# Performance work log

Hardware: AMD Instinct MI355X
Metric: run time of the kernel (lower is better)

The kernel has to match this reference:

```python
import jax, jax.numpy as jnp
import numpy as np

N_NODES = 100000
N_EDGES = 1600000
N_GRAPHS = 2048
F_IN = 33
D = 256


def _graph_conv(x, edge_index, w_rel, b_rel, w_root):
    # PyG GraphConv (aggr='add'): out = lin_rel(sum_j x_j) + lin_root(x)
    src, dst = edge_index[0], edge_index[1]
    agg = jax.ops.segment_sum(x[src], dst, num_segments=x.shape[0])  # [N, F]
    return agg @ w_rel + b_rel + x @ w_root


def setup_inputs() -> dict:
    key = jax.random.key(0)
    ks = jax.random.split(key, 16)
    scale_in = 1.0 / np.sqrt(F_IN)
    scale_d = 1.0 / np.sqrt(D)
    inp = {
        "x": jax.random.normal(ks[0], (N_NODES, F_IN), dtype=jnp.float32),
        "edge_index": jax.random.randint(ks[1], (2, N_EDGES), 0, N_NODES),
        "batch_index": jnp.sort(jax.random.randint(ks[2], (N_NODES,), 0, N_GRAPHS)),
        # initial_conv: GraphConv(F_IN -> D)
        "w_rel0": jax.random.normal(ks[3], (F_IN, D), dtype=jnp.float32) * scale_in,
        "b_rel0": jnp.zeros((D,), dtype=jnp.float32),
        "w_root0": jax.random.normal(ks[4], (F_IN, D), dtype=jnp.float32) * scale_in,
        # conv1..conv3: GraphConv(D -> D)
        "w_rel1": jax.random.normal(ks[5], (D, D), dtype=jnp.float32) * scale_d,
        "b_rel1": jnp.zeros((D,), dtype=jnp.float32),
        "w_root1": jax.random.normal(ks[6], (D, D), dtype=jnp.float32) * scale_d,
        "w_rel2": jax.random.normal(ks[7], (D, D), dtype=jnp.float32) * scale_d,
        "b_rel2": jnp.zeros((D,), dtype=jnp.float32),
        "w_root2": jax.random.normal(ks[8], (D, D), dtype=jnp.float32) * scale_d,
        "w_rel3": jax.random.normal(ks[9], (D, D), dtype=jnp.float32) * scale_d,
        "b_rel3": jnp.zeros((D,), dtype=jnp.float32),
        "w_root3": jax.random.normal(ks[10], (D, D), dtype=jnp.float32) * scale_d,
        # output head Linear(D -> 1)
        "w_out": jax.random.normal(ks[11], (D, 1), dtype=jnp.float32) * scale_d,
        "b_out": jnp.zeros((1,), dtype=jnp.float32),
    }
    return inp


def reference(x, edge_index, batch_index,
              w_rel0, b_rel0, w_root0,
              w_rel1, b_rel1, w_root1,
              w_rel2, b_rel2, w_root2,
              w_rel3, b_rel3, w_root3,
              w_out, b_out):
    # dropout omitted (eval mode)
    h = jax.nn.gelu(_graph_conv(x, edge_index, w_rel0, b_rel0, w_root0))
    h = jax.nn.gelu(_graph_conv(h, edge_index, w_rel1, b_rel1, w_root1))
    h = jax.nn.gelu(_graph_conv(h, edge_index, w_rel2, b_rel2, w_root2))
    h = jax.nn.gelu(_graph_conv(h, edge_index, w_rel3, b_rel3, w_root3))
    # global mean pool over graphs
    sums = jax.ops.segment_sum(h, batch_index, num_segments=N_GRAPHS)          # [G, D]
    counts = jax.ops.segment_sum(jnp.ones((h.shape[0],), h.dtype), batch_index,
                                 num_segments=N_GRAPHS)                         # [G]
    pooled = sums / jnp.maximum(counts, 1.0)[:, None]
    return pooled @ w_out + b_out                                               # [G, 1]
```

## Files before the change

kernel.cpp:

```cpp
#include <hip/hip_runtime.h>
#include <math.h>

#define NN 100000
#define NE 1600000
#define NG 2048
#define FIN 33
#define DD 256

#define SH 8
#define NB ((NN + 255) >> 8)
#define CH 4096
#define PCAP 4608
#define ESCAP 6144

typedef __attribute__((ext_vector_type(8))) short bf16x8;
typedef __attribute__((ext_vector_type(4))) float f32x4;

__device__ __forceinline__ float b2f(unsigned short u){
    union { unsigned int i; float f; } c; c.i = ((unsigned int)u) << 16; return c.f;
}
__device__ __forceinline__ unsigned short f2b(float f){
    union { float f; unsigned int u; } c; c.f = f;
    unsigned int r = c.u + 0x7fffu + ((c.u >> 16) & 1u);
    return (unsigned short)(r >> 16);
}

__device__ __forceinline__ float gelu_tanh(float x){
    float x3 = x * x * x;
    float t = tanhf(0.7978845608028654f * (x + 0.044715f * x3));
    return 0.5f * x * (1.0f + t);
}

__global__ __launch_bounds__(256) void k_bin(const int* __restrict__ src,
                                             const int* __restrict__ dst,
                                             int* __restrict__ gcur,
                                             int2* __restrict__ pairs){
    __shared__ int cnt[NB];
    __shared__ int lb[NB];
    __shared__ int gbase[NB];
    __shared__ int sc[512];
    __shared__ int2 stage[CH];

    int t = threadIdx.x;
    for(int i = t; i < NB; i += 256) cnt[i] = 0;
    __syncthreads();

    int e0 = blockIdx.x * CH;
    int n = NE - e0; if(n > CH) n = CH;

    int  myb[16];
    int  myr[16];
    int2 myp[16];
    #pragma unroll
    for(int k = 0; k < 16; k++){
        int e = e0 + t + k * 256;
        if(e < NE){
            int s = src[e], d = dst[e];
            int b = d >> SH;
            myr[k] = atomicAdd(&cnt[b], 1);
            myb[k] = b;
            myp[k] = make_int2(s, d);
        } else myb[k] = -1;
    }
    __syncthreads();

    sc[t]       = (t       < NB) ? cnt[t]       : 0;
    sc[t + 256] = (t + 256 < NB) ? cnt[t + 256] : 0;
    __syncthreads();
    for(int off = 1; off < 512; off <<= 1){
        int a  = (t >= off)       ? sc[t - off]       : 0;
        int b2 = (t + 256 >= off) ? sc[t + 256 - off] : 0;
        __syncthreads();
        sc[t] += a; sc[t + 256] += b2;
        __syncthreads();
    }
    for(int i = t; i < NB; i += 256){
        lb[i] = sc[i] - cnt[i];
        int c = cnt[i];
        gbase[i] = (c > 0) ? atomicAdd(&gcur[i], c) : 0;
    }
    __syncthreads();

    #pragma unroll
    for(int k = 0; k < 16; k++){
        if(myb[k] >= 0) stage[lb[myb[k]] + myr[k]] = myp[k];
    }
    __syncthreads();

    for(int i = t; i < n; i += 256){
        int2 p = stage[i];
        int b = p.y >> SH;
        int tgt = gbase[b] + (i - lb[b]);
        if(tgt < PCAP) pairs[(size_t)b * PCAP + tgt] = p;
    }
}

__global__ void k_sscan(const int* __restrict__ gcur, int* __restrict__ boff){
    __shared__ int s[512];
    int t = threadIdx.x;
    int v = 0;
    if(t < NB){ v = gcur[t]; if(v > PCAP) v = PCAP; }
    s[t] = v; __syncthreads();
    for(int off = 1; off < 512; off <<= 1){
        int u = (t >= off) ? s[t - off] : 0;
        __syncthreads();
        s[t] += u;
        __syncthreads();
    }
    if(t < NB) boff[t] = s[t] - v;
}

__global__ __launch_bounds__(256) void k_bcsr(const int2* __restrict__ pairs,
                                              const int* __restrict__ gcur,
                                              const int* __restrict__ boff,
                                              int* __restrict__ deg,
                                              int* __restrict__ rs,
                                              int* __restrict__ esrc){
    __shared__ int hist[256];
    __shared__ int sc[256];
    __shared__ int cur2[256];
    __shared__ int est[ESCAP];

    int b = blockIdx.x;
    int t = threadIdx.x;
    int m = gcur[b]; if(m > PCAP) m = PCAP;
    int pstart = boff[b];
    const int2* bp = pairs + (size_t)b * PCAP;

    hist[t] = 0;
    __syncthreads();
    for(int i = t; i < m; i += 256) atomicAdd(&hist[bp[i].y & 255], 1);
    __syncthreads();

    sc[t] = hist[t]; __syncthreads();
    for(int off = 1; off < 256; off <<= 1){
        int u = (t >= off) ? sc[t - off] : 0;
        __syncthreads();
        sc[t] += u;
        __syncthreads();
    }
    int excl = sc[t] - hist[t];
    cur2[t] = excl;
    int node = (b << 8) + t;
    if(node < NN){
        deg[node] = hist[t];
        rs[node]  = pstart + excl;
    }
    __syncthreads();

    for(int i = t; i < m; i += 256){
        int2 p = bp[i];
        int pos = atomicAdd(&cur2[p.y & 255], 1);
        if(pos < ESCAP) est[pos] = p.x;
        else esrc[pstart + pos] = p.x;
    }
    __syncthreads();
    int lim = (m < ESCAP) ? m : ESCAP;
    for(int i = t; i < lim; i += 256) esrc[pstart + i] = est[i];
}

__global__ void k_xpad(const float* __restrict__ x, unsigned short* __restrict__ xb){
    int idx = blockIdx.x * 256 + threadIdx.x;
    if(idx >= NN * 64) return;
    int n = idx >> 6, c = idx & 63;
    xb[idx] = (c < FIN) ? f2b(x[(size_t)n * FIN + c]) : 0;
}

__global__ void k_aggx(const unsigned short* __restrict__ xb, const int* __restrict__ rs,
                       const int* __restrict__ deg, const int* __restrict__ esrc,
                       unsigned short* __restrict__ axb){
    int wv = (blockIdx.x * blockDim.x + threadIdx.x) >> 6;
    int lane = threadIdx.x & 63;
    int node = wv * 4 + (lane >> 4);
    int l16 = lane & 15;
    if(node >= NN) return;
    int start = rs[node], cnt = deg[node];
    float a0 = 0.f, a1 = 0.f, a2 = 0.f, a3 = 0.f;
    const unsigned short* xp = xb + l16 * 4;
    int j = 0;
    for(; j + 4 <= cnt; j += 4){
        int e0 = esrc[start+j], e1 = esrc[start+j+1], e2 = esrc[start+j+2], e3 = esrc[start+j+3];
        ushort4 v0 = *(const ushort4*)(xp + (size_t)e0 * 64);
        ushort4 v1 = *(const ushort4*)(xp + (size_t)e1 * 64);
        ushort4 v2 = *(const ushort4*)(xp + (size_t)e2 * 64);
        ushort4 v3 = *(const ushort4*)(xp + (size_t)e3 * 64);
        a0 += (b2f(v0.x) + b2f(v1.x)) + (b2f(v2.x) + b2f(v3.x));
        a1 += (b2f(v0.y) + b2f(v1.y)) + (b2f(v2.y) + b2f(v3.y));
        a2 += (b2f(v0.z) + b2f(v1.z)) + (b2f(v2.z) + b2f(v3.z));
        a3 += (b2f(v0.w) + b2f(v1.w)) + (b2f(v2.w) + b2f(v3.w));
    }
    for(; j < cnt; j++){
        int e = esrc[start + j];
        ushort4 v = *(const ushort4*)(xp + (size_t)e * 64);
        a0 += b2f(v.x); a1 += b2f(v.y); a2 += b2f(v.z); a3 += b2f(v.w);
    }
    ushort4 o; o.x = f2b(a0); o.y = f2b(a1); o.z = f2b(a2); o.w = f2b(a3);
    *(ushort4*)(axb + (size_t)node * 64 + l16 * 4) = o;
}

__global__ void k_agg256(const unsigned short* __restrict__ h, const int* __restrict__ rs,
                         const int* __restrict__ deg, const int* __restrict__ esrc,
                         unsigned short* __restrict__ agg){
    int w = (blockIdx.x * blockDim.x + threadIdx.x) >> 6;
    int lane = threadIdx.x & 63;
    if(w >= NN) return;
    int start = rs[w], cnt = deg[w];
    float a0 = 0.f, a1 = 0.f, a2 = 0.f, a3 = 0.f;
    const unsigned short* hp = h + lane * 4;
    int j = 0;
    for(; j + 8 <= cnt; j += 8){
        int e0 = esrc[start+j+0], e1 = esrc[start+j+1], e2 = esrc[start+j+2], e3 = esrc[start+j+3];
        int e4 = esrc[start+j+4], e5 = esrc[start+j+5], e6 = esrc[start+j+6], e7 = esrc[start+j+7];
        ushort4 v0 = *(const ushort4*)(hp + (size_t)e0 * DD);
        ushort4 v1 = *(const ushort4*)(hp + (size_t)e1 * DD);
        ushort4 v2 = *(const ushort4*)(hp + (size_t)e2 * DD);
        ushort4 v3 = *(const ushort4*)(hp + (size_t)e3 * DD);
        ushort4 v4 = *(const ushort4*)(hp + (size_t)e4 * DD);
        ushort4 v5 = *(const ushort4*)(hp + (size_t)e5 * DD);
        ushort4 v6 = *(const ushort4*)(hp + (size_t)e6 * DD);
        ushort4 v7 = *(const ushort4*)(hp + (size_t)e7 * DD);
        a0 += ((b2f(v0.x)+b2f(v1.x)) + (b2f(v2.x)+b2f(v3.x))) + ((b2f(v4.x)+b2f(v5.x)) + (b2f(v6.x)+b2f(v7.x)));
        a1 += ((b2f(v0.y)+b2f(v1.y)) + (b2f(v2.y)+b2f(v3.y))) + ((b2f(v4.y)+b2f(v5.y)) + (b2f(v6.y)+b2f(v7.y)));
        a2 += ((b2f(v0.z)+b2f(v1.z)) + (b2f(v2.z)+b2f(v3.z))) + ((b2f(v4.z)+b2f(v5.z)) + (b2f(v6.z)+b2f(v7.z)));
        a3 += ((b2f(v0.w)+b2f(v1.w)) + (b2f(v2.w)+b2f(v3.w))) + ((b2f(v4.w)+b2f(v5.w)) + (b2f(v6.w)+b2f(v7.w)));
    }
    for(; j < cnt; j++){
        int s = esrc[start + j];
        ushort4 v = *(const ushort4*)(hp + (size_t)s * DD);
        a0 += b2f(v.x); a1 += b2f(v.y); a2 += b2f(v.z); a3 += b2f(v.w);
    }
    ushort4 o; o.x = f2b(a0); o.y = f2b(a1); o.z = f2b(a2); o.w = f2b(a3);
    *(ushort4*)(agg + (size_t)w * DD + lane * 4) = o;
}

__global__ void k_wt(const float* __restrict__ W, unsigned short* __restrict__ Bt){
    __shared__ float s[16][17];
    int tx = threadIdx.x, ty = threadIdx.y;
    int k = blockIdx.y * 16 + ty;
    int j = blockIdx.x * 16 + tx;
    s[ty][tx] = W[k * DD + j];
    __syncthreads();
    Bt[(size_t)(blockIdx.x * 16 + ty) * DD + blockIdx.y * 16 + tx] = f2b(s[tx][ty]);
}

__global__ void k_wt0(const float* __restrict__ W, unsigned short* __restrict__ Bt){
    int idx = blockIdx.x * 256 + threadIdx.x;
    if(idx >= DD * 64) return;
    int j = idx >> 6, k = idx & 63;
    Bt[idx] = (k < FIN) ? f2b(W[(size_t)k * DD + j]) : 0;
}

#define BMM 128
#define BNN 128
#define LPAD 40

template<int KS, int AST>
__global__ __launch_bounds__(256) void k_mfma_gemm(
    const unsigned short* __restrict__ A0, const unsigned short* __restrict__ A1,
    const unsigned short* __restrict__ Bt0, const unsigned short* __restrict__ Bt1,
    const float* __restrict__ bias, unsigned short* __restrict__ out)
{
    __shared__ unsigned short As[2][BMM * LPAD];
    __shared__ unsigned short Bs[2][BNN * LPAD];

    int t = threadIdx.x;
    int lane = t & 63;
    int w = t >> 6;
    int wm = (w >> 1) * 64;
    int wn = (w & 1) * 64;
    int i0 = blockIdx.x * BMM;
    int j0 = blockIdx.y * BNN;

    f32x4 acc[4][4];
    #pragma unroll
    for(int m = 0; m < 4; m++)
        #pragma unroll
        for(int n = 0; n < 4; n++)
            acc[m][n] = (f32x4){0.f, 0.f, 0.f, 0.f};

    int r16 = lane & 15;
    int kg  = lane >> 4;

    for(int os = 0; os < KS; os++){
        const unsigned short* Ap = (os < KS/2) ? A0 : A1;
        const unsigned short* Bp = (os < KS/2) ? Bt0 : Bt1;
        int kb = ((os < KS/2) ? os : os - KS/2) * 64;

        #pragma unroll
        for(int h = 0; h < 2; h++){
            int kk = kb + h * 32;
            #pragma unroll
            for(int p = 0; p < 2; p++){
                int idx = t + 256 * p;
                int row = idx >> 2;
                int seg = idx & 3;
                int gi = i0 + row;
                bf16x8 va = {};
                if(gi < NN) va = *(const bf16x8*)(Ap + (size_t)gi * AST + kk + seg * 8);
                *(bf16x8*)(&As[h][row * LPAD + seg * 8]) = va;
                bf16x8 vb = *(const bf16x8*)(Bp + (size_t)(j0 + row) * AST + kk + seg * 8);
                *(bf16x8*)(&Bs[h][row * LPAD + seg * 8]) = vb;
            }
        }
        __syncthreads();

        #pragma unroll
        for(int h = 0; h < 2; h++){
            bf16x8 af[4], bfr[4];
            #pragma unroll
            for(int m = 0; m < 4; m++)
                af[m] = *(const bf16x8*)(&As[h][(wm + m * 16 + r16) * LPAD + kg * 8]);
            #pragma unroll
            for(int n = 0; n < 4; n++)
                bfr[n] = *(const bf16x8*)(&Bs[h][(wn + n * 16 + r16) * LPAD + kg * 8]);
            #pragma unroll
            for(int m = 0; m < 4; m++)
                #pragma unroll
                for(int n = 0; n < 4; n++)
                    acc[m][n] = __builtin_amdgcn_mfma_f32_16x16x32_bf16(af[m], bfr[n], acc[m][n], 0, 0, 0);
        }
        __syncthreads();
    }

    int rg = kg * 4;
    #pragma unroll
    for(int n = 0; n < 4; n++){
        int gj = j0 + wn + n * 16 + r16;
        float bb = bias[gj];
        #pragma unroll
        for(int m = 0; m < 4; m++){
            #pragma unroll
            for(int r = 0; r < 4; r++){
                int gi = i0 + wm + m * 16 + rg + r;
                if(gi < NN)
                    out[(size_t)gi * DD + gj] = f2b(gelu_tanh(acc[m][n][r] + bb));
            }
        }
    }
}

__global__ void k_pool(const unsigned short* __restrict__ h, const int* __restrict__ batch,
                       const float* __restrict__ wout, float* __restrict__ gsum,
                       int* __restrict__ gcnt){
    int w = (blockIdx.x * blockDim.x + threadIdx.x) >> 6;
    int lane = threadIdx.x & 63;
    if(w >= NN) return;
    ushort4 hv = *(const ushort4*)(h + (size_t)w * DD + lane * 4);
    float4 wv = *(const float4*)(wout + lane * 4);
    float d = b2f(hv.x)*wv.x + b2f(hv.y)*wv.y + b2f(hv.z)*wv.z + b2f(hv.w)*wv.w;
    for(int off = 32; off > 0; off >>= 1) d += __shfl_down(d, off);
    if(lane == 0){
        int g = batch[w];
        atomicAdd(&gsum[g], d);
        atomicAdd(&gcnt[g], 1);
    }
}

__global__ void k_final(const float* __restrict__ gsum, const int* __restrict__ gcnt,
                        const float* __restrict__ bout, float* __restrict__ out){
    int g = blockIdx.x * 256 + threadIdx.x;
    if(g < NG) out[g] = gsum[g] / fmaxf((float)gcnt[g], 1.f) + bout[0];
}

extern "C" void kernel_launch(void* const* d_in, const int* in_sizes, int n_in,
                              void* d_out, int out_size, void* d_ws, size_t ws_size,
                              hipStream_t stream){
    const float* x       = (const float*)d_in[0];
    const int*   ei      = (const int*)d_in[1];
    const int*   src     = ei;
    const int*   dst     = ei + NE;
    const int*   batch   = (const int*)d_in[2];
    const float* w_rel0  = (const float*)d_in[3];
    const float* b_rel0  = (const float*)d_in[4];
    const float* w_root0 = (const float*)d_in[5];
    const float* w_rel1  = (const float*)d_in[6];
    const float* b_rel1  = (const float*)d_in[7];
    const float* w_root1 = (const float*)d_in[8];
    const float* w_rel2  = (const float*)d_in[9];
    const float* b_rel2  = (const float*)d_in[10];
    const float* w_root2 = (const float*)d_in[11];
    const float* w_rel3  = (const float*)d_in[12];
    const float* b_rel3  = (const float*)d_in[13];
    const float* w_root3 = (const float*)d_in[14];
    const float* w_out   = (const float*)d_in[15];
    const float* b_out   = (const float*)d_in[16];
    float* out = (float*)d_out;

    char* ws = (char*)d_ws;
    size_t off = 0;
    auto alloc = [&](size_t bytes) -> void* {
        void* p = ws + off;
        off = (off + bytes + 255) & ~(size_t)255;
        return p;
    };
    unsigned short* hA  = (unsigned short*)alloc((size_t)NN * DD * 2);
    unsigned short* hB  = (unsigned short*)alloc((size_t)NN * DD * 2);
    unsigned short* agg = (unsigned short*)alloc((size_t)NN * DD * 2);
    int*   deg  = (int*)alloc((size_t)NN * 4);
    int*   rs   = (int*)alloc((size_t)NN * 4);
    int*   esrc = (int*)alloc((size_t)NE * 4);
    int*   gcur = (int*)alloc(512 * 4);
    int*   boff = (int*)alloc(512 * 4);
    float* gsum = (float*)alloc((size_t)NG * 4);
    int*   gcnt = (int*)alloc((size_t)NG * 4);
    unsigned short* bt[6];
    for(int i = 0; i < 6; i++) bt[i] = (unsigned short*)alloc((size_t)DD * DD * 2);
    unsigned short* bt0r = (unsigned short*)alloc((size_t)DD * 64 * 2);
    unsigned short* bt0o = (unsigned short*)alloc((size_t)DD * 64 * 2);
    (void)ws_size; (void)in_sizes; (void)n_in; (void)out_size;

    int2* pairs = (int2*)hB;
    unsigned short* xb  = agg;
    unsigned short* axb = agg + (size_t)NN * 64 + 128;

    hipMemsetAsync(gcur, 0, 512 * 4, stream);
    k_bin<<<(NE + CH - 1) / CH, 256, 0, stream>>>(src, dst, gcur, pairs);
    k_sscan<<<1, 512, 0, stream>>>(gcur, boff);
    k_bcsr<<<NB, 256, 0, stream>>>(pairs, gcur, boff, deg, rs, esrc);

    dim3 wtg(16, 16), wtb(16, 16);
    k_wt<<<wtg, wtb, 0, stream>>>(w_rel1,  bt[0]);
    k_wt<<<wtg, wtb, 0, stream>>>(w_root1, bt[1]);
    k_wt<<<wtg, wtb, 0, stream>>>(w_rel2,  bt[2]);
    k_wt<<<wtg, wtb, 0, stream>>>(w_root2, bt[3]);
    k_wt<<<wtg, wtb, 0, stream>>>(w_rel3,  bt[4]);
    k_wt<<<wtg, wtb, 0, stream>>>(w_root3, bt[5]);
    k_wt0<<<(DD * 64 + 255) / 256, 256, 0, stream>>>(w_rel0,  bt0r);
    k_wt0<<<(DD * 64 + 255) / 256, 256, 0, stream>>>(w_root0, bt0o);
    k_xpad<<<(NN * 64 + 255) / 256, 256, 0, stream>>>(x, xb);

    int aggGrid = (NN + 3) / 4;
    int aggxGrid = (NN + 15) / 16;
    dim3 gg((NN + BMM - 1) / BMM, DD / BNN);

    k_aggx<<<aggxGrid, 256, 0, stream>>>(xb, rs, deg, esrc, axb);
    k_mfma_gemm<2, 64><<<gg, 256, 0, stream>>>(axb, xb, bt0r, bt0o, b_rel0, hA);
    k_agg256<<<aggGrid, 256, 0, stream>>>(hA, rs, deg, esrc, agg);
    k_mfma_gemm<8, 256><<<gg, 256, 0, stream>>>(agg, hA, bt[0], bt[1], b_rel1, hB);
    k_agg256<<<aggGrid, 256, 0, stream>>>(hB, rs, deg, esrc, agg);
    k_mfma_gemm<8, 256><<<gg, 256, 0, stream>>>(agg, hB, bt[2], bt[3], b_rel2, hA);
    k_agg256<<<aggGrid, 256, 0, stream>>>(hA, rs, deg, esrc, agg);
    k_mfma_gemm<8, 256><<<gg, 256, 0, stream>>>(agg, hA, bt[4], bt[5], b_rel3, hB);

    hipMemsetAsync(gsum, 0, (size_t)NG * 4, stream);
    hipMemsetAsync(gcnt, 0, (size_t)NG * 4, stream);
    k_pool<<<aggGrid, 256, 0, stream>>>(hB, batch, w_out, gsum, gcnt);
    k_final<<<(NG + 255) / 256, 256, 0, stream>>>(gsum, gcnt, b_out, out);
}
```

Before: 891.6 us.

## Vectorize 256-wide aggregation to two nodes per wave and double-buffer GEMM loads

```diff
diff --git a/kernel.cpp b/kernel.cpp
--- a/kernel.cpp
+++ b/kernel.cpp
@@ -201,36 +201,38 @@
 __global__ void k_agg256(const unsigned short* __restrict__ h, const int* __restrict__ rs,
                          const int* __restrict__ deg, const int* __restrict__ esrc,
                          unsigned short* __restrict__ agg){
-    int w = (blockIdx.x * blockDim.x + threadIdx.x) >> 6;
+    int wv = (blockIdx.x * blockDim.x + threadIdx.x) >> 6;
     int lane = threadIdx.x & 63;
-    if(w >= NN) return;
-    int start = rs[w], cnt = deg[w];
-    float a0 = 0.f, a1 = 0.f, a2 = 0.f, a3 = 0.f;
-    const unsigned short* hp = h + lane * 4;
+    int node = wv * 2 + (lane >> 5);
+    int l32 = lane & 31;
+    if(node >= NN) return;
+    int start = rs[node], cnt = deg[node];
+    float a[8] = {0.f,0.f,0.f,0.f,0.f,0.f,0.f,0.f};
+    const unsigned short* hp = h + l32 * 8;
     int j = 0;
     for(; j + 8 <= cnt; j += 8){
-        int e0 = esrc[start+j+0], e1 = esrc[start+j+1], e2 = esrc[start+j+2], e3 = esrc[start+j+3];
-        int e4 = esrc[start+j+4], e5 = esrc[start+j+5], e6 = esrc[start+j+6], e7 = esrc[start+j+7];
-        ushort4 v0 = *(const ushort4*)(hp + (size_t)e0 * DD);
-        ushort4 v1 = *(const ushort4*)(hp + (size_t)e1 * DD);
-        ushort4 v2 = *(const ushort4*)(hp + (size_t)e2 * DD);
-        ushort4 v3 = *(const ushort4*)(hp + (size_t)e3 * DD);
-        ushort4 v4 = *(const ushort4*)(hp + (size_t)e4 * DD);
-        ushort4 v5 = *(const ushort4*)(hp + (size_t)e5 * DD);
-        ushort4 v6 = *(const ushort4*)(hp + (size_t)e6 * DD);
-        ushort4 v7 = *(const ushort4*)(hp + (size_t)e7 * DD);
-        a0 += ((b2f(v0.x)+b2f(v1.x)) + (b2f(v2.x)+b2f(v3.x))) + ((b2f(v4.x)+b2f(v5.x)) + (b2f(v6.x)+b2f(v7.x)));
-        a1 += ((b2f(v0.y)+b2f(v1.y)) + (b2f(v2.y)+b2f(v3.y))) + ((b2f(v4.y)+b2f(v5.y)) + (b2f(v6.y)+b2f(v7.y)));
-        a2 += ((b2f(v0.z)+b2f(v1.z)) + (b2f(v2.z)+b2f(v3.z))) + ((b2f(v4.z)+b2f(v5.z)) + (b2f(v6.z)+b2f(v7.z)));
-        a3 += ((b2f(v0.w)+b2f(v1.w)) + (b2f(v2.w)+b2f(v3.w))) + ((b2f(v4.w)+b2f(v5.w)) + (b2f(v6.w)+b2f(v7.w)));
+        bf16x8 v[8];
+        #pragma unroll
+        for(int q = 0; q < 8; q++){
+            int e = esrc[start + j + q];
+            v[q] = *(const bf16x8*)(hp + (size_t)e * DD);
+        }
+        #pragma unroll
+        for(int q = 0; q < 8; q++)
+            #pragma unroll
+            for(int d = 0; d < 8; d++)
+                a[d] += b2f((unsigned short)v[q][d]);
     }
     for(; j < cnt; j++){
-        int s = esrc[start + j];
-        ushort4 v = *(const ushort4*)(hp + (size_t)s * DD);
-        a0 += b2f(v.x); a1 += b2f(v.y); a2 += b2f(v.z); a3 += b2f(v.w);
-    }
-    ushort4 o; o.x = f2b(a0); o.y = f2b(a1); o.z = f2b(a2); o.w = f2b(a3);
-    *(ushort4*)(agg + (size_t)w * DD + lane * 4) = o;
+        int e = esrc[start + j];
+        bf16x8 v = *(const bf16x8*)(hp + (size_t)e * DD);
+        #pragma unroll
+        for(int d = 0; d < 8; d++) a[d] += b2f((unsigned short)v[d]);
+    }
+    bf16x8 o;
+    #pragma unroll
+    for(int d = 0; d < 8; d++) o[d] = (short)f2b(a[d]);
+    *(bf16x8*)(agg + (size_t)node * DD + l32 * 8) = o;
 }
 
 __global__ void k_wt(const float* __restrict__ W, unsigned short* __restrict__ Bt){
@@ -271,6 +273,12 @@
     int i0 = blockIdx.x * BMM;
     int j0 = blockIdx.y * BNN;
 
+    int r16 = lane & 15;
+    int kg  = lane >> 4;
+
+    int srow0 = t >> 2,          sseg0 = (t & 3) * 8;
+    int srow1 = (t + 256) >> 2,  sseg1 = ((t + 256) & 3) * 8;
+
     f32x4 acc[4][4];
     #pragma unroll
     for(int m = 0; m < 4; m++)
@@ -278,48 +286,52 @@
         for(int n = 0; n < 4; n++)
             acc[m][n] = (f32x4){0.f, 0.f, 0.f, 0.f};
 
-    int r16 = lane & 15;
-    int kg  = lane >> 4;
-
-    for(int os = 0; os < KS; os++){
-        const unsigned short* Ap = (os < KS/2) ? A0 : A1;
-        const unsigned short* Bp = (os < KS/2) ? Bt0 : Bt1;
-        int kb = ((os < KS/2) ? os : os - KS/2) * 64;
-
-        #pragma unroll
-        for(int h = 0; h < 2; h++){
-            int kk = kb + h * 32;
-            #pragma unroll
-            for(int p = 0; p < 2; p++){
-                int idx = t + 256 * p;
-                int row = idx >> 2;
-                int seg = idx & 3;
-                int gi = i0 + row;
-                bf16x8 va = {};
-                if(gi < NN) va = *(const bf16x8*)(Ap + (size_t)gi * AST + kk + seg * 8);
-                *(bf16x8*)(&As[h][row * LPAD + seg * 8]) = va;
-                bf16x8 vb = *(const bf16x8*)(Bp + (size_t)(j0 + row) * AST + kk + seg * 8);
-                *(bf16x8*)(&Bs[h][row * LPAD + seg * 8]) = vb;
-            }
-        }
-        __syncthreads();
-
-        #pragma unroll
-        for(int h = 0; h < 2; h++){
-            bf16x8 af[4], bfr[4];
-            #pragma unroll
-            for(int m = 0; m < 4; m++)
-                af[m] = *(const bf16x8*)(&As[h][(wm + m * 16 + r16) * LPAD + kg * 8]);
+    const int steps = 2 * KS;
+
+    auto loadStep = [&](int s, bf16x8* va, bf16x8* vb){
+        const unsigned short* Ap = (s < KS) ? A0 : A1;
+        const unsigned short* Bp = (s < KS) ? Bt0 : Bt1;
+        int kk = ((s < KS) ? s : s - KS) * 32;
+        int gi0 = i0 + srow0, gi1 = i0 + srow1;
+        va[0] = (bf16x8){};
+        va[1] = (bf16x8){};
+        if(gi0 < NN) va[0] = *(const bf16x8*)(Ap + (size_t)gi0 * AST + kk + sseg0);
+        if(gi1 < NN) va[1] = *(const bf16x8*)(Ap + (size_t)gi1 * AST + kk + sseg1);
+        vb[0] = *(const bf16x8*)(Bp + (size_t)(j0 + srow0) * AST + kk + sseg0);
+        vb[1] = *(const bf16x8*)(Bp + (size_t)(j0 + srow1) * AST + kk + sseg1);
+    };
+    auto writeStep = [&](int buf, const bf16x8* va, const bf16x8* vb){
+        *(bf16x8*)(&As[buf][srow0 * LPAD + sseg0]) = va[0];
+        *(bf16x8*)(&As[buf][srow1 * LPAD + sseg1]) = va[1];
+        *(bf16x8*)(&Bs[buf][srow0 * LPAD + sseg0]) = vb[0];
+        *(bf16x8*)(&Bs[buf][srow1 * LPAD + sseg1]) = vb[1];
+    };
+
+    bf16x8 va[2], vb[2], va2[2], vb2[2];
+    loadStep(0, va, vb);
+    writeStep(0, va, vb);
+    int cur = 0;
+
+    for(int s = 0; s < steps; s++){
+        bool more = (s + 1 < steps);
+        if(more) loadStep(s + 1, va2, vb2);
+        __syncthreads();
+
+        bf16x8 af[4], bfr[4];
+        #pragma unroll
+        for(int m = 0; m < 4; m++)
+            af[m] = *(const bf16x8*)(&As[cur][(wm + m * 16 + r16) * LPAD + kg * 8]);
+        #pragma unroll
+        for(int n = 0; n < 4; n++)
+            bfr[n] = *(const bf16x8*)(&Bs[cur][(wn + n * 16 + r16) * LPAD + kg * 8]);
+        #pragma unroll
+        for(int m = 0; m < 4; m++)
             #pragma unroll
             for(int n = 0; n < 4; n++)
-                bfr[n] = *(const bf16x8*)(&Bs[h][(wn + n * 16 + r16) * LPAD + kg * 8]);
-            #pragma unroll
-            for(int m = 0; m < 4; m++)
-                #pragma unroll
-                for(int n = 0; n < 4; n++)
-                    acc[m][n] = __builtin_amdgcn_mfma_f32_16x16x32_bf16(af[m], bfr[n], acc[m][n], 0, 0, 0);
-        }
-        __syncthreads();
+                acc[m][n] = __builtin_amdgcn_mfma_f32_16x16x32_bf16(af[m], bfr[n], acc[m][n], 0, 0, 0);
+
+        if(more) writeStep(cur ^ 1, va2, vb2);
+        cur ^= 1;
     }
 
     int rg = kg * 4;
@@ -429,17 +441,17 @@
     k_wt0<<<(DD * 64 + 255) / 256, 256, 0, stream>>>(w_root0, bt0o);
     k_xpad<<<(NN * 64 + 255) / 256, 256, 0, stream>>>(x, xb);
 
-    int aggGrid = (NN + 3) / 4;
-    int aggxGrid = (NN + 15) / 16;
+    int aggGrid  = (NN + 3) / 4;
+    int agg2Grid = (NN * 32 + 255) / 256;
     dim3 gg((NN + BMM - 1) / BMM, DD / BNN);
 
-    k_aggx<<<aggxGrid, 256, 0, stream>>>(xb, rs, deg, esrc, axb);
+    k_aggx<<<(NN + 15) / 16, 256, 0, stream>>>(xb, rs, deg, esrc, axb);
     k_mfma_gemm<2, 64><<<gg, 256, 0, stream>>>(axb, xb, bt0r, bt0o, b_rel0, hA);
-    k_agg256<<<aggGrid, 256, 0, stream>>>(hA, rs, deg, esrc, agg);
+    k_agg256<<<agg2Grid, 256, 0, stream>>>(hA, rs, deg, esrc, agg);
     k_mfma_gemm<8, 256><<<gg, 256, 0, stream>>>(agg, hA, bt[0], bt[1], b_rel1, hB);
-    k_agg256<<<aggGrid, 256, 0, stream>>>(hB, rs, deg, esrc, agg);
+    k_agg256<<<agg2Grid, 256, 0, stream>>>(hB, rs, deg, esrc, agg);
     k_mfma_gemm<8, 256><<<gg, 256, 0, stream>>>(agg, hB, bt[2], bt[3], b_rel2, hA);
-    k_agg256<<<aggGrid, 256, 0, stream>>>(hA, rs, deg, esrc, agg);
+    k_agg256<<<agg2Grid, 256, 0, stream>>>(hA, rs, deg, esrc, agg);
     k_mfma_gemm<8, 256><<<gg, 256, 0, stream>>>(agg, hA, bt[4], bt[5], b_rel3, hB);
 
     hipMemsetAsync(gsum, 0, (size_t)NG * 4, stream);
```

Result: slower. 910.7 us (+2.1%).
